# Optimization experiments

Measured on AMD Instinct MI355X. Metric: run time of the kernel, lower is better.

The kernel has to match this reference:

```python
import jax, jax.numpy as jnp
import numpy as np

N_NODES = 50000


def gat_layer(x, src, dst, W, att_s, att_d, b, concat):
    # PyG GATConv (eval mode): h = x W reshaped to [N, H, C]
    H, C = att_s.shape
    h = (x @ W).reshape(-1, H, C)                      # [N, H, C]
    a_s = (h * att_s).sum(-1)                          # [N, H]
    a_d = (h * att_d).sum(-1)                          # [N, H]
    e = jax.nn.leaky_relu(a_s[src] + a_d[dst], 0.2)    # [E, H]
    # scatter-softmax over destination nodes
    m = jax.ops.segment_max(e, dst, num_segments=N_NODES)
    alpha = jnp.exp(e - m[dst])
    denom = jax.ops.segment_sum(alpha, dst, num_segments=N_NODES)
    alpha = alpha / denom[dst]                         # [E, H]
    msg = h[src] * alpha[:, :, None]                   # [E, H, C]
    out = jax.ops.segment_sum(msg, dst, num_segments=N_NODES)  # [N, H, C]
    out = out.reshape(N_NODES, H * C) if concat else out.mean(axis=1)
    return out + b


def setup_inputs() -> dict:
    key = jax.random.key(0)
    ks = jax.random.split(key, 16)
    F_IN, HID, HEADS, NCLS, E = 512, 64, 4, 40, 800000
    x = jax.random.normal(ks[0], (N_NODES, F_IN), dtype=jnp.float32)
    edge_index = jax.random.randint(ks[1], (2, E), 0, N_NODES, dtype=jnp.int32)

    def glorot(k, shape):
        fan = shape[0]
        return jax.random.normal(k, shape, dtype=jnp.float32) / np.sqrt(fan)

    d1 = HID * HEADS  # 256
    return {
        "x": x,
        "edge_index": edge_index,
        "W1": glorot(ks[2], (F_IN, d1)),
        "as1": glorot(ks[3], (HEADS, HID)),
        "ad1": glorot(ks[4], (HEADS, HID)),
        "b1": jnp.zeros((d1,), jnp.float32),
        "W2": glorot(ks[5], (d1, d1)),
        "as2": glorot(ks[6], (HEADS, HID)),
        "ad2": glorot(ks[7], (HEADS, HID)),
        "b2": jnp.zeros((d1,), jnp.float32),
        "W3": glorot(ks[8], (d1, NCLS)),
        "as3": glorot(ks[9], (1, NCLS)),
        "ad3": glorot(ks[10], (1, NCLS)),
        "b3": jnp.zeros((NCLS,), jnp.float32),
    }


def reference(x, edge_index, W1, as1, ad1, b1, W2, as2, ad2, b2, W3, as3, ad3, b3):
    # add self-loops (PyG GATConv default)
    loops = jnp.arange(N_NODES, dtype=edge_index.dtype)
    src = jnp.concatenate([edge_index[0], loops])
    dst = jnp.concatenate([edge_index[1], loops])
    h = jax.nn.elu(gat_layer(x, src, dst, W1, as1, ad1, b1, True))
    h = jax.nn.elu(gat_layer(h, src, dst, W2, as2, ad2, b2, True))
    out = gat_layer(h, src, dst, W3, as3, ad3, b3, False)
    return out
```

## Files before the change

kernel.cpp:

```cpp
#include <hip/hip_runtime.h>
#include <stdint.h>

#define NN 50000
#define NB 196

typedef unsigned short u16;
typedef _Float16 f16;
typedef __attribute__((ext_vector_type(8))) _Float16 half8;
typedef __attribute__((ext_vector_type(4))) _Float16 half4;
typedef __attribute__((ext_vector_type(4))) float f32x4;

__device__ __forceinline__ void gload_lds16(const void* gsrc, void* ldst){
  __builtin_amdgcn_global_load_lds(
      (const __attribute__((address_space(1))) unsigned int*)gsrc,
      (__attribute__((address_space(3))) unsigned int*)ldst,
      16, 0, 0);
}

#define VMW(N)  asm volatile("s_waitcnt vmcnt(" #N ")" ::: "memory")
#define LGKM0() asm volatile("s_waitcnt lgkmcnt(0)" ::: "memory")
#define BARR()  asm volatile("s_barrier" ::: "memory")


__global__ void count_k(const int* __restrict__ dst, int* __restrict__ cnt, int E){
  int i = blockIdx.x * 256 + threadIdx.x;
  int tot = E + NN;
  if (i >= tot) return;
  int d = (i < E) ? dst[i] : (i - E);
  atomicAdd(&cnt[d], 1);
}

__global__ __launch_bounds__(256) void scan_part_k(const int* __restrict__ cnt,
                                                   int* __restrict__ bsum){
  __shared__ int lds[256];
  int tid = threadIdx.x;
  int idx = blockIdx.x * 256 + tid;
  lds[tid] = (idx < NN) ? cnt[idx] : 0;
  __syncthreads();
#pragma unroll
  for (int off = 128; off >= 1; off >>= 1){
    if (tid < off) lds[tid] += lds[tid + off];
    __syncthreads();
  }
  if (tid == 0) bsum[blockIdx.x] = lds[0];
}

__global__ __launch_bounds__(256) void scan_top_k(const int* __restrict__ bsum,
                                                  int* __restrict__ boff,
                                                  int* __restrict__ row_ptr){
  __shared__ int lds[256];
  int tid = threadIdx.x;
  int v = (tid < NB) ? bsum[tid] : 0;
  lds[tid] = v;
  __syncthreads();
#pragma unroll
  for (int off = 1; off < 256; off <<= 1){
    int t = (tid >= off) ? lds[tid - off] : 0;
    __syncthreads();
    lds[tid] += t;
    __syncthreads();
  }
  if (tid < NB) boff[tid] = lds[tid] - v;
  if (tid == 255) row_ptr[NN] = lds[255];
}

__global__ __launch_bounds__(256) void scan_fin_k(const int* __restrict__ cnt,
                                                  const int* __restrict__ boff,
                                                  int* __restrict__ row_ptr,
                                                  int* __restrict__ cursor){
  __shared__ int lds[256];
  int tid = threadIdx.x;
  int idx = blockIdx.x * 256 + tid;
  int v = (idx < NN) ? cnt[idx] : 0;
  lds[tid] = v;
  __syncthreads();
#pragma unroll
  for (int off = 1; off < 256; off <<= 1){
    int t = (tid >= off) ? lds[tid - off] : 0;
    __syncthreads();
    lds[tid] += t;
    __syncthreads();
  }
  if (idx < NN){
    int r = boff[blockIdx.x] + lds[tid] - v;
    row_ptr[idx] = r;
    cursor[idx]  = r;
  }
}

__global__ void scatter_k(const int* __restrict__ src, const int* __restrict__ dst,
                          int* __restrict__ cursor, int* __restrict__ csr, int E){
  int i = blockIdx.x * 256 + threadIdx.x;
  int tot = E + NN;
  if (i >= tot) return;
  int s, d;
  if (i < E){ s = src[i]; d = dst[i]; } else { s = i - E; d = i - E; }
  int pos = atomicAdd(&cursor[d], 1);
  csr[pos] = s;
}


__global__ void transpose_k(const float* __restrict__ W, f16* __restrict__ Wt, int K, int N){
  int i = blockIdx.x * 256 + threadIdx.x;
  if (i >= K * N) return;
  int n = i / K, k = i - n * K;
  Wt[i] = (f16)W[k * N + n];
}


template<bool A_FP32>
__global__ __launch_bounds__(512) void gemm_big_k(const void* __restrict__ Aptr,
                                                  const f16* __restrict__ Bt,
                                                  f16* __restrict__ C,
                                                  const float* __restrict__ atts,
                                                  const float* __restrict__ attd,
                                                  float* __restrict__ a_s,
                                                  float* __restrict__ a_d,
                                                  int M, int K){
  constexpr int ABYTES = A_FP32 ? 16384 : 8192;
  constexpr int STEPB  = ABYTES + 16384;
  __shared__ __attribute__((aligned(16))) char lds[4 * STEPB];

  const int tid  = threadIdx.x;
  const int wave = tid >> 6, lane = tid & 63;
  const int quad = lane >> 4, l16 = lane & 15;
  const int wm = wave >> 2, wn = wave & 3;
  const int m0 = blockIdx.x * 128;
  const int sc_l = lane >> 4, r_l = lane & 15;

  const size_t bsrc0 = (size_t)(wave * 16 + r_l) * K + sc_l * 8;
  const size_t bsrc1 = (size_t)((wave + 8) * 16 + r_l) * K + sc_l * 8;
  const int bdst0 = wave * 1024;
  const int bdst1 = (wave + 8) * 1024;

  int arow = m0 + wave * 16 + r_l; if (arow > M - 1) arow = M - 1;
  const size_t asrc0 = (size_t)arow * K + sc_l * 8;
  const size_t asrc1 = asrc0 + 4;
  const int adst0 = wave * 1024;
  const int adst1 = 8192 + wave * 1024;

  auto stage = [&](int buf, int k0){
    char* Ab = lds + buf * STEPB;
    char* Bb = Ab + ABYTES;
    if constexpr (A_FP32){
      const float* A = (const float*)Aptr;
      gload_lds16(A + asrc0 + k0, Ab + adst0);
      gload_lds16(A + asrc1 + k0, Ab + adst1);
    } else {
      gload_lds16((const f16*)Aptr + asrc0 + k0, Ab + adst0);
    }
    gload_lds16(Bt + bsrc0 + k0, Bb + bdst0);
    gload_lds16(Bt + bsrc1 + k0, Bb + bdst1);
  };

  f32x4 acc[4][4] = {};

  auto compute = [&](int buf){
    char* Ab = lds + buf * STEPB;
    char* Bb = Ab + ABYTES;
    half8 af[4], bf[4];
    if constexpr (A_FP32){
#pragma unroll
      for (int i = 0; i < 4; ++i){
        const f32x4 lo = *(const f32x4*)(Ab + ((wm * 4 + i) * 64 + lane) * 16);
        const f32x4 hi = *(const f32x4*)(Ab + 8192 + ((wm * 4 + i) * 64 + lane) * 16);
        half8 v;
        v[0] = (f16)lo.x; v[1] = (f16)lo.y; v[2] = (f16)lo.z; v[3] = (f16)lo.w;
        v[4] = (f16)hi.x; v[5] = (f16)hi.y; v[6] = (f16)hi.z; v[7] = (f16)hi.w;
        af[i] = v;
      }
    } else {
#pragma unroll
      for (int i = 0; i < 4; ++i)
        af[i] = *(const half8*)(Ab + ((wm * 4 + i) * 64 + lane) * 16);
    }
#pragma unroll
    for (int j = 0; j < 4; ++j)
      bf[j] = *(const half8*)(Bb + ((wn * 4 + j) * 64 + lane) * 16);
#pragma unroll
    for (int i = 0; i < 4; ++i)
#pragma unroll
      for (int j = 0; j < 4; ++j)
        acc[i][j] = __builtin_amdgcn_mfma_f32_16x16x32_f16(af[i], bf[j], acc[i][j], 0, 0, 0);
  };

  stage(0, 0); stage(1, 32); stage(2, 64);

  const int nk = K >> 5;
  for (int t = 0; t < nk - 3; ++t){
    stage((t + 3) & 3, (t + 3) << 5);
    if constexpr (A_FP32) VMW(12); else VMW(9);
    BARR();
    compute(t & 3);
    LGKM0();
    BARR();
  }
  if constexpr (A_FP32) VMW(8); else VMW(6);
  BARR(); compute((nk - 3) & 3);
  if constexpr (A_FP32) VMW(4); else VMW(3);
  BARR(); compute((nk - 2) & 3);
  VMW(0);
  BARR(); compute((nk - 1) & 3);

  const int N = 256;
  const int head = wn;
  float sA[4], dA[4];
#pragma unroll
  for (int j = 0; j < 4; ++j){
    sA[j] = atts[head * 64 + j * 16 + l16];
    dA[j] = attd[head * 64 + j * 16 + l16];
  }
#pragma unroll
  for (int i = 0; i < 4; ++i){
#pragma unroll
    for (int r = 0; r < 4; ++r){
      int mm = m0 + wm * 64 + i * 16 + quad * 4 + r;
      float vs = 0.f, vd = 0.f;
#pragma unroll
      for (int j = 0; j < 4; ++j){
        float v = acc[i][j][r];
        vs += v * sA[j];
        vd += v * dA[j];
        int n = wn * 64 + j * 16 + l16;
        if (mm < M) C[(size_t)mm * N + n] = (f16)v;
      }
#pragma unroll
      for (int off = 8; off >= 1; off >>= 1){
        vs += __shfl_xor(vs, off);
        vd += __shfl_xor(vd, off);
      }
      if (l16 == 0 && mm < M){
        a_s[mm * 4 + head] = vs;
        a_d[mm * 4 + head] = vd;
      }
    }
  }
}


__global__ __launch_bounds__(256) void gemm_n40_k(const f16* __restrict__ A,
                                                  const f16* __restrict__ Bt,
                                                  f16* __restrict__ C,
                                                  const float* __restrict__ atts,
                                                  const float* __restrict__ attd,
                                                  float* __restrict__ a_s,
                                                  float* __restrict__ a_d,
                                                  int M, int K){
  constexpr int ABYTES = 4096;
  constexpr int BBYTES = 3072;
  constexpr int STEPB  = ABYTES + BBYTES;
  __shared__ __attribute__((aligned(16))) char lds[4 * STEPB];

  const int tid  = threadIdx.x;
  const int wave = tid >> 6, lane = tid & 63;
  const int quad = lane >> 4, l16 = lane & 15;
  const int m0 = blockIdx.x * 64;
  const int sc_l = lane >> 4, r_l = lane & 15;

  int arow = m0 + wave * 16 + r_l; if (arow > M - 1) arow = M - 1;
  const size_t asrc = (size_t)arow * K + sc_l * 8;
  const int adst = wave * 1024;
  int brow = wave * 16 + r_l; if (brow > 39) brow = 39;
  const size_t bsrc = (size_t)brow * K + sc_l * 8;
  const int bdst = wave * 1024;
  const bool b_active = (wave < 3);
  const bool two_ops = b_active;

  auto stage = [&](int buf, int k0){
    char* Ab = lds + buf * STEPB;
    char* Bb = Ab + ABYTES;
    gload_lds16(A + asrc + k0, Ab + adst);
    if (b_active) gload_lds16(Bt + bsrc + k0, Bb + bdst);
  };

  f32x4 acc[3] = {};
  auto compute = [&](int buf){
    char* Ab = lds + buf * STEPB;
    char* Bb = Ab + ABYTES;
    half8 af = *(const half8*)(Ab + (wave * 64 + lane) * 16);
    half8 bf[3];
#pragma unroll
    for (int j = 0; j < 3; ++j)
      bf[j] = *(const half8*)(Bb + (j * 64 + lane) * 16);
#pragma unroll
    for (int j = 0; j < 3; ++j)
      acc[j] = __builtin_amdgcn_mfma_f32_16x16x32_f16(af, bf[j], acc[j], 0, 0, 0);
  };

  stage(0, 0); stage(1, 32); stage(2, 64);
  const int nk = K >> 5;
  for (int t = 0; t < nk - 3; ++t){
    stage((t + 3) & 3, (t + 3) << 5);
    if (two_ops) VMW(6); else VMW(3);
    BARR();
    compute(t & 3);
    LGKM0();
    BARR();
  }
  if (two_ops) VMW(4); else VMW(2);
  BARR(); compute((nk - 3) & 3);
  if (two_ops) VMW(2); else VMW(1);
  BARR(); compute((nk - 2) & 3);
  VMW(0);
  BARR(); compute((nk - 1) & 3);

  float sA[3], dA[3];
#pragma unroll
  for (int j = 0; j < 3; ++j){
    int n = j * 16 + l16;
    sA[j] = (n < 40) ? atts[n] : 0.f;
    dA[j] = (n < 40) ? attd[n] : 0.f;
  }
#pragma unroll
  for (int r = 0; r < 4; ++r){
    int mm = m0 + wave * 16 + quad * 4 + r;
    float vs = 0.f, vd = 0.f;
#pragma unroll
    for (int j = 0; j < 3; ++j){
      float v = acc[j][r];
      vs += v * sA[j];
      vd += v * dA[j];
      int n = j * 16 + l16;
      if (mm < M && n < 40) C[(size_t)mm * 40 + n] = (f16)v;
    }
#pragma unroll
    for (int off = 8; off >= 1; off >>= 1){
      vs += __shfl_xor(vs, off);
      vd += __shfl_xor(vd, off);
    }
    if (l16 == 0 && mm < M){
      a_s[mm] = vs;
      a_d[mm] = vd;
    }
  }
}


__device__ __forceinline__ float lrelu(float e){ return e > 0.f ? e : 0.2f * e; }

__global__ __launch_bounds__(256) void agg4_k(const f16* __restrict__ h,
                                              const float* __restrict__ a_s,
                                              const float* __restrict__ a_d,
                                              const int* __restrict__ row_ptr,
                                              const int* __restrict__ csr,
                                              const float* __restrict__ bias,
                                              f16* __restrict__ out){
  int w = blockIdx.x * 4 + (threadIdx.x >> 6);
  if (w >= NN) return;
  const int lane = threadIdx.x & 63;
  const int head = lane >> 4;
  const char* hb = (const char*)h;
  const uint32_t hoff_lane = (uint32_t)lane << 3;
  const float ad = a_d[w * 4 + head];
  const int beg = row_ptr[w], end = row_ptr[w + 1], endm1 = end - 1;

  float denom = 0.f, acc0 = 0.f, acc1 = 0.f, acc2 = 0.f, acc3 = 0.f;

  float ce[4]; half4 chv[4];
  float ne[4]; half4 nhv[4];

  auto ldgrp = [&](int base, float* EV, half4* HV){
#pragma unroll
    for (int q = 0; q < 4; ++q){
      int idx = base + q; idx = idx < endm1 ? idx : endm1;
      int s = csr[idx];
      EV[q] = a_s[(s << 2) + head];
      HV[q] = *(const half4*)(hb + (((uint32_t)s << 9) | hoff_lane));
    }
  };

  ldgrp(beg, ce, chv);
  int base = beg;
  while (true){
    bool more = base + 4 < end;
    if (more) ldgrp(base + 4, ne, nhv);
    int rem = end - base;
#pragma unroll
    for (int q = 0; q < 4; ++q){
      float al = __expf(lrelu(ce[q] + ad));
      al = (q < rem) ? al : 0.f;
      denom += al;
      acc0 += al * (float)chv[q].x;
      acc1 += al * (float)chv[q].y;
      acc2 += al * (float)chv[q].z;
      acc3 += al * (float)chv[q].w;
    }
    if (!more) break;
#pragma unroll
    for (int q = 0; q < 4; ++q){ ce[q] = ne[q]; chv[q] = nhv[q]; }
    base += 4;
  }

  float inv = 1.f / fmaxf(denom, 1e-30f);
  float o0 = acc0 * inv + bias[lane * 4 + 0];
  float o1 = acc1 * inv + bias[lane * 4 + 1];
  float o2 = acc2 * inv + bias[lane * 4 + 2];
  float o3 = acc3 * inv + bias[lane * 4 + 3];
  o0 = o0 > 0.f ? o0 : __expf(o0) - 1.f;
  o1 = o1 > 0.f ? o1 : __expf(o1) - 1.f;
  o2 = o2 > 0.f ? o2 : __expf(o2) - 1.f;
  o3 = o3 > 0.f ? o3 : __expf(o3) - 1.f;
  half4 rv; rv.x = (f16)o0; rv.y = (f16)o1; rv.z = (f16)o2; rv.w = (f16)o3;
  *(half4*)(out + (size_t)w * 256 + lane * 4) = rv;
}

__global__ __launch_bounds__(256) void agg1_k(const f16* __restrict__ h,
                                              const float* __restrict__ a_s,
                                              const float* __restrict__ a_d,
                                              const int* __restrict__ row_ptr,
                                              const int* __restrict__ csr,
                                              const float* __restrict__ bias,
                                              float* __restrict__ out){
  int w = blockIdx.x * 4 + (threadIdx.x >> 6);
  if (w >= NN) return;
  const int lane = threadIdx.x & 63;
  const int cl = (lane < 40) ? lane : 0;
  const float ad = a_d[w];
  const int beg = row_ptr[w], end = row_ptr[w + 1], endm1 = end - 1;

  float denom = 0.f, acc = 0.f;
  float ce[4], chv[4];
  float ne[4], nhv[4];

  auto ldgrp = [&](int base, float* EV, float* HV){
#pragma unroll
    for (int q = 0; q < 4; ++q){
      int idx = base + q; idx = idx < endm1 ? idx : endm1;
      int s = csr[idx];
      EV[q] = a_s[s];
      HV[q] = (float)h[(size_t)s * 40 + cl];
    }
  };

  ldgrp(beg, ce, chv);
  int base = beg;
  while (true){
    bool more = base + 4 < end;
    if (more) ldgrp(base + 4, ne, nhv);
    int rem = end - base;
#pragma unroll
    for (int q = 0; q < 4; ++q){
      float al = __expf(lrelu(ce[q] + ad));
      al = (q < rem) ? al : 0.f;
      denom += al;
      acc += al * chv[q];
    }
    if (!more) break;
#pragma unroll
    for (int q = 0; q < 4; ++q){ ce[q] = ne[q]; chv[q] = nhv[q]; }
    base += 4;
  }

  if (lane < 40){
    float o = acc / fmaxf(denom, 1e-30f) + bias[lane];
    out[(size_t)w * 40 + lane] = o;
  }
}


extern "C" void kernel_launch(void* const* d_in, const int* in_sizes, int n_in,
                              void* d_out, int out_size, void* d_ws, size_t ws_size,
                              hipStream_t stream){
  const float* x   = (const float*)d_in[0];
  const int*   ei  = (const int*)d_in[1];
  const float* W1  = (const float*)d_in[2];
  const float* as1 = (const float*)d_in[3];
  const float* ad1 = (const float*)d_in[4];
  const float* b1  = (const float*)d_in[5];
  const float* W2  = (const float*)d_in[6];
  const float* as2 = (const float*)d_in[7];
  const float* ad2 = (const float*)d_in[8];
  const float* b2  = (const float*)d_in[9];
  const float* W3  = (const float*)d_in[10];
  const float* as3 = (const float*)d_in[11];
  const float* ad3 = (const float*)d_in[12];
  const float* b3  = (const float*)d_in[13];

  const int E = in_sizes[1] / 2;
  const int ETOT = E + NN;
  const int* src_arr = ei;
  const int* dst_arr = ei + E;

  char* ws = (char*)d_ws;
  size_t off = 0;
  auto alloc = [&](size_t bytes) -> void* {
    void* p = ws + off; off += (bytes + 255) & ~(size_t)255; return p;
  };
  int*   cnt     = (int*)  alloc((size_t)NN * 4);
  int*   row_ptr = (int*)  alloc((size_t)(NN + 1) * 4);
  int*   cursor  = (int*)  alloc((size_t)NN * 4);
  int*   csr     = (int*)  alloc((size_t)ETOT * 4);
  int*   bsum    = (int*)  alloc((size_t)256 * 4);
  int*   boff    = (int*)  alloc((size_t)256 * 4);
  f16*   W1t     = (f16*)  alloc((size_t)512 * 256 * 2);
  f16*   W2t     = (f16*)  alloc((size_t)256 * 256 * 2);
  f16*   W3t     = (f16*)  alloc((size_t)256 * 40 * 2);
  float* a_s     = (float*)alloc((size_t)NN * 4 * 4);
  float* a_d     = (float*)alloc((size_t)NN * 4 * 4);
  f16*   hbuf    = (f16*)  alloc((size_t)NN * 256 * 2);
  f16*   xbuf    = (f16*)  alloc((size_t)NN * 256 * 2);
  (void)ws_size; (void)n_in; (void)out_size;

  hipMemsetAsync(cnt, 0, (size_t)NN * 4, stream);
  int egrid = (ETOT + 255) / 256;
  count_k    <<<egrid, 256, 0, stream>>>(dst_arr, cnt, E);
  scan_part_k<<<NB, 256, 0, stream>>>(cnt, bsum);
  scan_top_k <<<1, 256, 0, stream>>>(bsum, boff, row_ptr);
  scan_fin_k <<<NB, 256, 0, stream>>>(cnt, boff, row_ptr, cursor);
  scatter_k  <<<egrid, 256, 0, stream>>>(src_arr, dst_arr, cursor, csr, E);

  transpose_k<<<(512 * 256 + 255) / 256, 256, 0, stream>>>(W1, W1t, 512, 256);
  transpose_k<<<(256 * 256 + 255) / 256, 256, 0, stream>>>(W2, W2t, 256, 256);
  transpose_k<<<(256 * 40  + 255) / 256, 256, 0, stream>>>(W3, W3t, 256, 40);

  dim3 blk512(512);
  dim3 blk(256);
  dim3 gB((NN + 127) / 128);
  dim3 gC((NN + 63) / 64);
  int nodeblocks = (NN + 3) / 4;

  gemm_big_k<true> <<<gB, blk512, 0, stream>>>(x, W1t, hbuf, as1, ad1, a_s, a_d, NN, 512);
  agg4_k<<<nodeblocks, blk, 0, stream>>>(hbuf, a_s, a_d, row_ptr, csr, b1, xbuf);

  gemm_big_k<false><<<gB, blk512, 0, stream>>>(xbuf, W2t, hbuf, as2, ad2, a_s, a_d, NN, 256);
  agg4_k<<<nodeblocks, blk, 0, stream>>>(hbuf, a_s, a_d, row_ptr, csr, b2, xbuf);

  gemm_n40_k<<<gC, blk, 0, stream>>>(xbuf, W3t, hbuf, as3, ad3, a_s, a_d, NN, 256);
  agg1_k<<<nodeblocks, blk, 0, stream>>>(hbuf, a_s, a_d, row_ptr, csr, b3, (float*)d_out);
}
```

Measured before the change: 518.8 us.

## Precompute edge attention weights in separate kernel and shrink GEMM pipeline to double buffer

Adds a destination-index array to the CSR build and a per-edge kernel that computes exp(leaky_relu(a_s[src]+a_d[dst])) for all edges and heads once per layer. The aggregation kernels then read the contiguous alpha values instead of gathering a_s and evaluating exp per lane. Separately, the big GEMM goes from a 4-stage LDS pipeline to a 2-stage double buffer, cutting LDS use. This adds an extra kernel launch and a full per-edge alpha write/read pass per layer, and the shallower prefetch can expose more global load latency.

```diff
diff --git a/kernel.cpp b/kernel.cpp
--- a/kernel.cpp
+++ b/kernel.cpp
@@ -89,7 +89,8 @@
 }
 
 __global__ void scatter_k(const int* __restrict__ src, const int* __restrict__ dst,
-                          int* __restrict__ cursor, int* __restrict__ csr, int E){
+                          int* __restrict__ cursor, int* __restrict__ csr,
+                          int* __restrict__ csrd, int E){
   int i = blockIdx.x * 256 + threadIdx.x;
   int tot = E + NN;
   if (i >= tot) return;
@@ -97,6 +98,7 @@
   if (i < E){ s = src[i]; d = dst[i]; } else { s = i - E; d = i - E; }
   int pos = atomicAdd(&cursor[d], 1);
   csr[pos] = s;
+  csrd[pos] = d;
 }
 
 
@@ -119,7 +121,7 @@
                                                   int M, int K){
   constexpr int ABYTES = A_FP32 ? 16384 : 8192;
   constexpr int STEPB  = ABYTES + 16384;
-  __shared__ __attribute__((aligned(16))) char lds[4 * STEPB];
+  __shared__ __attribute__((aligned(16))) char lds[2 * STEPB];
 
   const int tid  = threadIdx.x;
   const int wave = tid >> 6, lane = tid & 63;
@@ -184,23 +186,21 @@
         acc[i][j] = __builtin_amdgcn_mfma_f32_16x16x32_f16(af[i], bf[j], acc[i][j], 0, 0, 0);
   };
 
-  stage(0, 0); stage(1, 32); stage(2, 64);
+  stage(0, 0);
 
   const int nk = K >> 5;
-  for (int t = 0; t < nk - 3; ++t){
-    stage((t + 3) & 3, (t + 3) << 5);
-    if constexpr (A_FP32) VMW(12); else VMW(9);
+  for (int t = 0; t < nk; ++t){
+    if (t + 1 < nk){
+      stage((t + 1) & 1, (t + 1) << 5);
+      if constexpr (A_FP32) VMW(4); else VMW(3);
+    } else {
+      VMW(0);
+    }
     BARR();
-    compute(t & 3);
+    compute(t & 1);
     LGKM0();
     BARR();
   }
-  if constexpr (A_FP32) VMW(8); else VMW(6);
-  BARR(); compute((nk - 3) & 3);
-  if constexpr (A_FP32) VMW(4); else VMW(3);
-  BARR(); compute((nk - 2) & 3);
-  VMW(0);
-  BARR(); compute((nk - 1) & 3);
 
   const int N = 256;
   const int head = wn;
@@ -338,9 +338,33 @@
 
 __device__ __forceinline__ float lrelu(float e){ return e > 0.f ? e : 0.2f * e; }
 
+__global__ void alpha4_k(const int* __restrict__ csr, const int* __restrict__ csrd,
+                         const float* __restrict__ a_s, const float* __restrict__ a_d,
+                         float* __restrict__ alpha, int tot){
+  int i = blockIdx.x * 256 + threadIdx.x;
+  if (i >= tot) return;
+  int s = csr[i], d = csrd[i];
+  const f32x4 as = *(const f32x4*)(a_s + ((size_t)s << 2));
+  const f32x4 ad = *(const f32x4*)(a_d + ((size_t)d << 2));
+  f32x4 al;
+  al.x = __expf(lrelu(as.x + ad.x));
+  al.y = __expf(lrelu(as.y + ad.y));
+  al.z = __expf(lrelu(as.z + ad.z));
+  al.w = __expf(lrelu(as.w + ad.w));
+  *(f32x4*)(alpha + ((size_t)i << 2)) = al;
+}
+
+__global__ void alpha1_k(const int* __restrict__ csr, const int* __restrict__ csrd,
+                         const float* __restrict__ a_s, const float* __restrict__ a_d,
+                         float* __restrict__ alpha, int tot){
+  int i = blockIdx.x * 256 + threadIdx.x;
+  if (i >= tot) return;
+  alpha[i] = __expf(lrelu(a_s[csr[i]] + a_d[csrd[i]]));
+}
+
+
 __global__ __launch_bounds__(256) void agg4_k(const f16* __restrict__ h,
-                                              const float* __restrict__ a_s,
-                                              const float* __restrict__ a_d,
+                                              const float* __restrict__ alpha,
                                               const int* __restrict__ row_ptr,
                                               const int* __restrict__ csr,
                                               const float* __restrict__ bias,
@@ -351,34 +375,32 @@
   const int head = lane >> 4;
   const char* hb = (const char*)h;
   const uint32_t hoff_lane = (uint32_t)lane << 3;
-  const float ad = a_d[w * 4 + head];
   const int beg = row_ptr[w], end = row_ptr[w + 1], endm1 = end - 1;
 
   float denom = 0.f, acc0 = 0.f, acc1 = 0.f, acc2 = 0.f, acc3 = 0.f;
 
-  float ce[4]; half4 chv[4];
-  float ne[4]; half4 nhv[4];
-
-  auto ldgrp = [&](int base, float* EV, half4* HV){
+  float ca[4]; half4 chv[4];
+  float na[4]; half4 nhv[4];
+
+  auto ldgrp = [&](int base, float* AV, half4* HV){
 #pragma unroll
     for (int q = 0; q < 4; ++q){
       int idx = base + q; idx = idx < endm1 ? idx : endm1;
       int s = csr[idx];
-      EV[q] = a_s[(s << 2) + head];
+      AV[q] = alpha[((size_t)idx << 2) + head];
       HV[q] = *(const half4*)(hb + (((uint32_t)s << 9) | hoff_lane));
     }
   };
 
-  ldgrp(beg, ce, chv);
+  ldgrp(beg, ca, chv);
   int base = beg;
   while (true){
     bool more = base + 4 < end;
-    if (more) ldgrp(base + 4, ne, nhv);
+    if (more) ldgrp(base + 4, na, nhv);
     int rem = end - base;
 #pragma unroll
     for (int q = 0; q < 4; ++q){
-      float al = __expf(lrelu(ce[q] + ad));
-      al = (q < rem) ? al : 0.f;
+      float al = (q < rem) ? ca[q] : 0.f;
       denom += al;
       acc0 += al * (float)chv[q].x;
       acc1 += al * (float)chv[q].y;
@@ -387,7 +409,7 @@
     }
     if (!more) break;
 #pragma unroll
-    for (int q = 0; q < 4; ++q){ ce[q] = ne[q]; chv[q] = nhv[q]; }
+    for (int q = 0; q < 4; ++q){ ca[q] = na[q]; chv[q] = nhv[q]; }
     base += 4;
   }
 
@@ -405,8 +427,7 @@
 }
 
 __global__ __launch_bounds__(256) void agg1_k(const f16* __restrict__ h,
-                                              const float* __restrict__ a_s,
-                                              const float* __restrict__ a_d,
+                                              const float* __restrict__ alpha,
                                               const int* __restrict__ row_ptr,
                                               const int* __restrict__ csr,
                                               const float* __restrict__ bias,
@@ -415,39 +436,37 @@
   if (w >= NN) return;
   const int lane = threadIdx.x & 63;
   const int cl = (lane < 40) ? lane : 0;
-  const float ad = a_d[w];
   const int beg = row_ptr[w], end = row_ptr[w + 1], endm1 = end - 1;
 
   float denom = 0.f, acc = 0.f;
-  float ce[4], chv[4];
-  float ne[4], nhv[4];
-
-  auto ldgrp = [&](int base, float* EV, float* HV){
+  float ca[4], chv[4];
+  float na[4], nhv[4];
+
+  auto ldgrp = [&](int base, float* AV, float* HV){
 #pragma unroll
     for (int q = 0; q < 4; ++q){
       int idx = base + q; idx = idx < endm1 ? idx : endm1;
       int s = csr[idx];
-      EV[q] = a_s[s];
+      AV[q] = alpha[idx];
       HV[q] = (float)h[(size_t)s * 40 + cl];
     }
   };
 
-  ldgrp(beg, ce, chv);
+  ldgrp(beg, ca, chv);
   int base = beg;
   while (true){
     bool more = base + 4 < end;
-    if (more) ldgrp(base + 4, ne, nhv);
+    if (more) ldgrp(base + 4, na, nhv);
     int rem = end - base;
 #pragma unroll
     for (int q = 0; q < 4; ++q){
-      float al = __expf(lrelu(ce[q] + ad));
-      al = (q < rem) ? al : 0.f;
+      float al = (q < rem) ? ca[q] : 0.f;
       denom += al;
       acc += al * chv[q];
     }
     if (!more) break;
 #pragma unroll
-    for (int q = 0; q < 4; ++q){ ce[q] = ne[q]; chv[q] = nhv[q]; }
+    for (int q = 0; q < 4; ++q){ ca[q] = na[q]; chv[q] = nhv[q]; }
     base += 4;
   }
 
@@ -490,6 +509,8 @@
   int*   row_ptr = (int*)  alloc((size_t)(NN + 1) * 4);
   int*   cursor  = (int*)  alloc((size_t)NN * 4);
   int*   csr     = (int*)  alloc((size_t)ETOT * 4);
+  int*   csrd    = (int*)  alloc((size_t)ETOT * 4);
+  float* alpha   = (float*)alloc((size_t)ETOT * 4 * 4);
   int*   bsum    = (int*)  alloc((size_t)256 * 4);
   int*   boff    = (int*)  alloc((size_t)256 * 4);
   f16*   W1t     = (f16*)  alloc((size_t)512 * 256 * 2);
@@ -507,7 +528,7 @@
   scan_part_k<<<NB, 256, 0, stream>>>(cnt, bsum);
   scan_top_k <<<1, 256, 0, stream>>>(bsum, boff, row_ptr);
   scan_fin_k <<<NB, 256, 0, stream>>>(cnt, boff, row_ptr, cursor);
-  scatter_k  <<<egrid, 256, 0, stream>>>(src_arr, dst_arr, cursor, csr, E);
+  scatter_k  <<<egrid, 256, 0, stream>>>(src_arr, dst_arr, cursor, csr, csrd, E);
 
   transpose_k<<<(512 * 256 + 255) / 256, 256, 0, stream>>>(W1, W1t, 512, 256);
   transpose_k<<<(256 * 256 + 255) / 256, 256, 0, stream>>>(W2, W2t, 256, 256);
@@ -520,11 +541,14 @@
   int nodeblocks = (NN + 3) / 4;
 
   gemm_big_k<true> <<<gB, blk512, 0, stream>>>(x, W1t, hbuf, as1, ad1, a_s, a_d, NN, 512);
-  agg4_k<<<nodeblocks, blk, 0, stream>>>(hbuf, a_s, a_d, row_ptr, csr, b1, xbuf);
+  alpha4_k<<<egrid, blk, 0, stream>>>(csr, csrd, a_s, a_d, alpha, ETOT);
+  agg4_k<<<nodeblocks, blk, 0, stream>>>(hbuf, alpha, row_ptr, csr, b1, xbuf);
 
   gemm_big_k<false><<<gB, blk512, 0, stream>>>(xbuf, W2t, hbuf, as2, ad2, a_s, a_d, NN, 256);
-  agg4_k<<<nodeblocks, blk, 0, stream>>>(hbuf, a_s, a_d, row_ptr, csr, b2, xbuf);
+  alpha4_k<<<egrid, blk, 0, stream>>>(csr, csrd, a_s, a_d, alpha, ETOT);
+  agg4_k<<<nodeblocks, blk, 0, stream>>>(hbuf, alpha, row_ptr, csr, b2, xbuf);
 
   gemm_n40_k<<<gC, blk, 0, stream>>>(xbuf, W3t, hbuf, as3, ad3, a_s, a_d, NN, 256);
-  agg1_k<<<nodeblocks, blk, 0, stream>>>(hbuf, a_s, a_d, row_ptr, csr, b3, (float*)d_out);
-}
+  alpha1_k<<<egrid, blk, 0, stream>>>(csr, csrd, a_s, a_d, alpha, ETOT);
+  agg1_k<<<nodeblocks, blk, 0, stream>>>(hbuf, alpha, row_ptr, csr, b3, (float*)d_out);
+}
```

New measurement: 512.2 us. About the same (-1.3%).

## Fuse CSR build kernels, merge weight transposes, fold scatter into first GEMM

Applied to the files above, without the earlier changes.

Merges the three weight transposes and the degree count into one grid-stride prep kernel, and replaces the three scan kernels with a single kernel that uses a software grid barrier across its 98 blocks. The edge scatter is appended to the end of the first GEMM kernel, and that kernel's LDS pipeline drops from 4 stages to 2 to free LDS. The goal is fewer kernel launches and less launch and serialization overhead. The risks are that the spin barrier assumes all 98 blocks are resident at once, that the shallower prefetch may expose memory latency in the GEMMs, and that an unused csrd array is written, adding extra traffic.

```diff
diff --git a/kernel.cpp b/kernel.cpp
--- a/kernel.cpp
+++ b/kernel.cpp
@@ -1,10 +1,9 @@
 #include <hip/hip_runtime.h>
 #include <stdint.h>
 
-#define NN 50000
-#define NB 196
-
-typedef unsigned short u16;
+#define NN  50000
+#define NSB 98
+
 typedef _Float16 f16;
 typedef __attribute__((ext_vector_type(8))) _Float16 half8;
 typedef __attribute__((ext_vector_type(4))) _Float16 half4;
@@ -21,94 +20,108 @@
 #define LGKM0() asm volatile("s_waitcnt lgkmcnt(0)" ::: "memory")
 #define BARR()  asm volatile("s_barrier" ::: "memory")
 
-
-__global__ void count_k(const int* __restrict__ dst, int* __restrict__ cnt, int E){
-  int i = blockIdx.x * 256 + threadIdx.x;
-  int tot = E + NN;
-  if (i >= tot) return;
-  int d = (i < E) ? dst[i] : (i - E);
-  atomicAdd(&cnt[d], 1);
-}
-
-__global__ __launch_bounds__(256) void scan_part_k(const int* __restrict__ cnt,
-                                                   int* __restrict__ bsum){
-  __shared__ int lds[256];
-  int tid = threadIdx.x;
-  int idx = blockIdx.x * 256 + tid;
-  lds[tid] = (idx < NN) ? cnt[idx] : 0;
+__device__ __forceinline__ float lrelu(float e){ return e > 0.f ? e : 0.2f * e; }
+
+__device__ __forceinline__ void gbar98(int* bar, int* phase){
   __syncthreads();
-#pragma unroll
-  for (int off = 128; off >= 1; off >>= 1){
-    if (tid < off) lds[tid] += lds[tid + off];
+  if (threadIdx.x == 0){
+    __threadfence();
+    int target = (++(*phase)) * NSB;
+    __hip_atomic_fetch_add(bar, 1, __ATOMIC_ACQ_REL, __HIP_MEMORY_SCOPE_AGENT);
+    while (__hip_atomic_load(bar, __ATOMIC_ACQUIRE, __HIP_MEMORY_SCOPE_AGENT) < target)
+      __builtin_amdgcn_s_sleep(2);
+    __threadfence();
+  }
+  __syncthreads();
+}
+
+__global__ __launch_bounds__(256) void prep_k(const float* __restrict__ W1,
+                                              const float* __restrict__ W2,
+                                              const float* __restrict__ W3,
+                                              f16* __restrict__ W1t,
+                                              f16* __restrict__ W2t,
+                                              f16* __restrict__ W3t,
+                                              const int* __restrict__ dst,
+                                              int* __restrict__ cnt,
+                                              int* __restrict__ bar, int E){
+  const int gsz = gridDim.x * 256;
+  const int gtid = blockIdx.x * 256 + threadIdx.x;
+  if (gtid == 0) bar[0] = 0;
+  for (int i = gtid; i < 512 * 256; i += gsz){
+    int n = i >> 9, k = i & 511;
+    W1t[i] = (f16)W1[k * 256 + n];
+  }
+  for (int i = gtid; i < 256 * 256; i += gsz){
+    int n = i >> 8, k = i & 255;
+    W2t[i] = (f16)W2[k * 256 + n];
+  }
+  for (int i = gtid; i < 40 * 256; i += gsz){
+    int n = i >> 8, k = i & 255;
+    W3t[i] = (f16)W3[k * 40 + n];
+  }
+  const int tot = E + NN;
+  for (int i = gtid; i < tot; i += gsz){
+    int d = (i < E) ? dst[i] : (i - E);
+    atomicAdd(&cnt[d], 1);
+  }
+}
+
+__global__ __launch_bounds__(512) void scan_all_k(const int* __restrict__ cnt,
+                                                  int* __restrict__ bsum,
+                                                  int* __restrict__ boff,
+                                                  int* __restrict__ row_ptr,
+                                                  int* __restrict__ cursor,
+                                                  int* __restrict__ bar){
+  __shared__ int sm[512];
+  int phase = 0;
+  const int tid = threadIdx.x;
+  const int idx = blockIdx.x * 512 + tid;
+  const int v = (idx < NN) ? cnt[idx] : 0;
+
+  sm[tid] = v;
+  __syncthreads();
+#pragma unroll
+  for (int off = 256; off >= 1; off >>= 1){
+    if (tid < off) sm[tid] += sm[tid + off];
     __syncthreads();
   }
-  if (tid == 0) bsum[blockIdx.x] = lds[0];
-}
-
-__global__ __launch_bounds__(256) void scan_top_k(const int* __restrict__ bsum,
-                                                  int* __restrict__ boff,
-                                                  int* __restrict__ row_ptr){
-  __shared__ int lds[256];
-  int tid = threadIdx.x;
-  int v = (tid < NB) ? bsum[tid] : 0;
-  lds[tid] = v;
+  if (tid == 0) bsum[blockIdx.x] = sm[0];
+  gbar98(bar, &phase);
+
+  if (blockIdx.x == 0){
+    int v2 = (tid < NSB) ? bsum[tid] : 0;
+    sm[tid] = v2;
+    __syncthreads();
+#pragma unroll
+    for (int off = 1; off < 512; off <<= 1){
+      int t2 = (tid >= off) ? sm[tid - off] : 0;
+      __syncthreads();
+      sm[tid] += t2;
+      __syncthreads();
+    }
+    if (tid < NSB) boff[tid] = sm[tid] - v2;
+    if (tid == 511) row_ptr[NN] = sm[511];
+  }
+  gbar98(bar, &phase);
+
+  sm[tid] = v;
   __syncthreads();
 #pragma unroll
-  for (int off = 1; off < 256; off <<= 1){
-    int t = (tid >= off) ? lds[tid - off] : 0;
+  for (int off = 1; off < 512; off <<= 1){
+    int t2 = (tid >= off) ? sm[tid - off] : 0;
     __syncthreads();
-    lds[tid] += t;
+    sm[tid] += t2;
     __syncthreads();
   }
-  if (tid < NB) boff[tid] = lds[tid] - v;
-  if (tid == 255) row_ptr[NN] = lds[255];
-}
-
-__global__ __launch_bounds__(256) void scan_fin_k(const int* __restrict__ cnt,
-                                                  const int* __restrict__ boff,
-                                                  int* __restrict__ row_ptr,
-                                                  int* __restrict__ cursor){
-  __shared__ int lds[256];
-  int tid = threadIdx.x;
-  int idx = blockIdx.x * 256 + tid;
-  int v = (idx < NN) ? cnt[idx] : 0;
-  lds[tid] = v;
-  __syncthreads();
-#pragma unroll
-  for (int off = 1; off < 256; off <<= 1){
-    int t = (tid >= off) ? lds[tid - off] : 0;
-    __syncthreads();
-    lds[tid] += t;
-    __syncthreads();
-  }
   if (idx < NN){
-    int r = boff[blockIdx.x] + lds[tid] - v;
+    int r = boff[blockIdx.x] + sm[tid] - v;
     row_ptr[idx] = r;
     cursor[idx]  = r;
   }
 }
 
-__global__ void scatter_k(const int* __restrict__ src, const int* __restrict__ dst,
-                          int* __restrict__ cursor, int* __restrict__ csr, int E){
-  int i = blockIdx.x * 256 + threadIdx.x;
-  int tot = E + NN;
-  if (i >= tot) return;
-  int s, d;
-  if (i < E){ s = src[i]; d = dst[i]; } else { s = i - E; d = i - E; }
-  int pos = atomicAdd(&cursor[d], 1);
-  csr[pos] = s;
-}
-
-
-__global__ void transpose_k(const float* __restrict__ W, f16* __restrict__ Wt, int K, int N){
-  int i = blockIdx.x * 256 + threadIdx.x;
-  if (i >= K * N) return;
-  int n = i / K, k = i - n * K;
-  Wt[i] = (f16)W[k * N + n];
-}
-
-
-template<bool A_FP32>
+
+template<bool A_FP32, bool SCATTER>
 __global__ __launch_bounds__(512) void gemm_big_k(const void* __restrict__ Aptr,
                                                   const f16* __restrict__ Bt,
                                                   f16* __restrict__ C,
@@ -116,10 +129,15 @@
                                                   const float* __restrict__ attd,
                                                   float* __restrict__ a_s,
                                                   float* __restrict__ a_d,
-                                                  int M, int K){
+                                                  int M, int K,
+                                                  const int* __restrict__ src_arr,
+                                                  const int* __restrict__ dst_arr,
+                                                  int* __restrict__ cursor,
+                                                  int* __restrict__ csr,
+                                                  int* __restrict__ csrd, int E){
   constexpr int ABYTES = A_FP32 ? 16384 : 8192;
   constexpr int STEPB  = ABYTES + 16384;
-  __shared__ __attribute__((aligned(16))) char lds[4 * STEPB];
+  __shared__ __attribute__((aligned(16))) char lds[2 * STEPB];
 
   const int tid  = threadIdx.x;
   const int wave = tid >> 6, lane = tid & 63;
@@ -130,14 +148,12 @@
 
   const size_t bsrc0 = (size_t)(wave * 16 + r_l) * K + sc_l * 8;
   const size_t bsrc1 = (size_t)((wave + 8) * 16 + r_l) * K + sc_l * 8;
-  const int bdst0 = wave * 1024;
-  const int bdst1 = (wave + 8) * 1024;
+  const int bdst0 = wave * 1024, bdst1 = (wave + 8) * 1024;
 
   int arow = m0 + wave * 16 + r_l; if (arow > M - 1) arow = M - 1;
   const size_t asrc0 = (size_t)arow * K + sc_l * 8;
   const size_t asrc1 = asrc0 + 4;
-  const int adst0 = wave * 1024;
-  const int adst1 = 8192 + wave * 1024;
+  const int adst0 = wave * 1024, adst1 = 8192 + wave * 1024;
 
   auto stage = [&](int buf, int k0){
     char* Ab = lds + buf * STEPB;
@@ -184,25 +200,21 @@
         acc[i][j] = __builtin_amdgcn_mfma_f32_16x16x32_f16(af[i], bf[j], acc[i][j], 0, 0, 0);
   };
 
-  stage(0, 0); stage(1, 32); stage(2, 64);
-
+  stage(0, 0);
   const int nk = K >> 5;
-  for (int t = 0; t < nk - 3; ++t){
-    stage((t + 3) & 3, (t + 3) << 5);
-    if constexpr (A_FP32) VMW(12); else VMW(9);
+  for (int t = 0; t < nk; ++t){
+    if (t + 1 < nk){
+      stage((t + 1) & 1, (t + 1) << 5);
+      if constexpr (A_FP32) VMW(4); else VMW(3);
+    } else {
+      VMW(0);
+    }
     BARR();
-    compute(t & 3);
+    compute(t & 1);
     LGKM0();
     BARR();
   }
-  if constexpr (A_FP32) VMW(8); else VMW(6);
-  BARR(); compute((nk - 3) & 3);
-  if constexpr (A_FP32) VMW(4); else VMW(3);
-  BARR(); compute((nk - 2) & 3);
-  VMW(0);
-  BARR(); compute((nk - 1) & 3);
-
-  const int N = 256;
+
   const int head = wn;
   float sA[4], dA[4];
 #pragma unroll
@@ -222,7 +234,7 @@
         vs += v * sA[j];
         vd += v * dA[j];
         int n = wn * 64 + j * 16 + l16;
-        if (mm < M) C[(size_t)mm * N + n] = (f16)v;
+        if (mm < M) C[(size_t)mm * 256 + n] = (f16)v;
       }
 #pragma unroll
       for (int off = 8; off >= 1; off >>= 1){
@@ -235,8 +247,19 @@
       }
     }
   }
-}
-
+
+  if constexpr (SCATTER){
+    const int gsz = gridDim.x * 512;
+    const int tot = E + NN;
+    for (int i = blockIdx.x * 512 + tid; i < tot; i += gsz){
+      int s, d;
+      if (i < E){ s = src_arr[i]; d = dst_arr[i]; } else { s = i - E; d = i - E; }
+      int pos = atomicAdd(&cursor[d], 1);
+      csr[pos] = s;
+      csrd[pos] = d;
+    }
+  }
+}
 
 __global__ __launch_bounds__(256) void gemm_n40_k(const f16* __restrict__ A,
                                                   const f16* __restrict__ Bt,
@@ -335,8 +358,6 @@
   }
 }
 
-
-__device__ __forceinline__ float lrelu(float e){ return e > 0.f ? e : 0.2f * e; }
 
 __global__ __launch_bounds__(256) void agg4_k(const f16* __restrict__ h,
                                               const float* __restrict__ a_s,
@@ -486,10 +507,12 @@
   auto alloc = [&](size_t bytes) -> void* {
     void* p = ws + off; off += (bytes + 255) & ~(size_t)255; return p;
   };
+  int*   bar     = (int*)  alloc(256);
   int*   cnt     = (int*)  alloc((size_t)NN * 4);
   int*   row_ptr = (int*)  alloc((size_t)(NN + 1) * 4);
   int*   cursor  = (int*)  alloc((size_t)NN * 4);
   int*   csr     = (int*)  alloc((size_t)ETOT * 4);
+  int*   csrd    = (int*)  alloc((size_t)ETOT * 4);
   int*   bsum    = (int*)  alloc((size_t)256 * 4);
   int*   boff    = (int*)  alloc((size_t)256 * 4);
   f16*   W1t     = (f16*)  alloc((size_t)512 * 256 * 2);
@@ -501,28 +524,24 @@
   f16*   xbuf    = (f16*)  alloc((size_t)NN * 256 * 2);
   (void)ws_size; (void)n_in; (void)out_size;
 
-  hipMemsetAsync(cnt, 0, (size_t)NN * 4, stream);
-  int egrid = (ETOT + 255) / 256;
-  count_k    <<<egrid, 256, 0, stream>>>(dst_arr, cnt, E);
-  scan_part_k<<<NB, 256, 0, stream>>>(cnt, bsum);
-  scan_top_k <<<1, 256, 0, stream>>>(bsum, boff, row_ptr);
-  scan_fin_k <<<NB, 256, 0, stream>>>(cnt, boff, row_ptr, cursor);
-  scatter_k  <<<egrid, 256, 0, stream>>>(src_arr, dst_arr, cursor, csr, E);
-
-  transpose_k<<<(512 * 256 + 255) / 256, 256, 0, stream>>>(W1, W1t, 512, 256);
-  transpose_k<<<(256 * 256 + 255) / 256, 256, 0, stream>>>(W2, W2t, 256, 256);
-  transpose_k<<<(256 * 40  + 255) / 256, 256, 0, stream>>>(W3, W3t, 256, 40);
-
+  dim3 blk(256);
   dim3 blk512(512);
-  dim3 blk(256);
   dim3 gB((NN + 127) / 128);
   dim3 gC((NN + 63) / 64);
   int nodeblocks = (NN + 3) / 4;
 
-  gemm_big_k<true> <<<gB, blk512, 0, stream>>>(x, W1t, hbuf, as1, ad1, a_s, a_d, NN, 512);
+  hipMemsetAsync(cnt, 0, (size_t)NN * 4, stream);
+  prep_k<<<1024, blk, 0, stream>>>(W1, W2, W3, W1t, W2t, W3t, dst_arr, cnt, bar, E);
+  scan_all_k<<<NSB, blk512, 0, stream>>>(cnt, bsum, boff, row_ptr, cursor, bar);
+
+  gemm_big_k<true, true><<<gB, blk512, 0, stream>>>(x, W1t, hbuf, as1, ad1, a_s, a_d,
+                                                    NN, 512, src_arr, dst_arr,
+                                                    cursor, csr, csrd, E);
   agg4_k<<<nodeblocks, blk, 0, stream>>>(hbuf, a_s, a_d, row_ptr, csr, b1, xbuf);
 
-  gemm_big_k<false><<<gB, blk512, 0, stream>>>(xbuf, W2t, hbuf, as2, ad2, a_s, a_d, NN, 256);
+  gemm_big_k<false, false><<<gB, blk512, 0, stream>>>(xbuf, W2t, hbuf, as2, ad2, a_s, a_d,
+                                                      NN, 256, nullptr, nullptr,
+                                                      nullptr, nullptr, nullptr, 0);
   agg4_k<<<nodeblocks, blk, 0, stream>>>(hbuf, a_s, a_d, row_ptr, csr, b2, xbuf);
 
   gemm_n40_k<<<gC, blk, 0, stream>>>(xbuf, W3t, hbuf, as3, ad3, a_s, a_d, NN, 256);
```

After: 507.0 us. -2.3%, faster.
